# Kernel optimization log

Hardware: AMD Instinct MI355X
Metric: run time of the kernel (lower is better)

## Reference

```python
import jax, jax.numpy as jnp
import numpy as np

D, H, E, K, DFF = 1024, 16, 8, 2, 4096
B, L, T = 4, 512, 2048
EPS = 1e-5


def _xavier(key, shape):
    fan_in, fan_out = shape[-1], shape[-2]
    a = jnp.sqrt(6.0 / (fan_in + fan_out))
    return jax.random.uniform(key, shape, jnp.float32, -a, a)


def setup_inputs() -> dict:
    key = jax.random.key(0)
    ks = jax.random.split(key, 16)
    inp = {
        'latents': jax.random.normal(ks[0], (B, L, D), jnp.float32),
        'tokens': jax.random.normal(ks[1], (B, T, D), jnp.float32),
        # self-attn
        'sa_ln_g': jnp.ones((D,)), 'sa_ln_b': jnp.zeros((D,)),
        'sa_in_w': _xavier(ks[2], (3 * D, D)), 'sa_in_b': jnp.zeros((3 * D,)),
        'sa_out_w': _xavier(ks[3], (D, D)), 'sa_out_b': jnp.zeros((D,)),
        # cross-attn
        'ca_q_ln_g': jnp.ones((D,)), 'ca_q_ln_b': jnp.zeros((D,)),
        'ca_kv_ln_g': jnp.ones((D,)), 'ca_kv_ln_b': jnp.zeros((D,)),
        'ca_in_w': _xavier(ks[4], (3 * D, D)), 'ca_in_b': jnp.zeros((3 * D,)),
        'ca_out_w': _xavier(ks[5], (D, D)), 'ca_out_b': jnp.zeros((D,)),
        # FuseMoE
        'moe_ln_g': jnp.ones((D,)), 'moe_ln_b': jnp.zeros((D,)),
        'router_w': _xavier(ks[6], (E, D)), 'router_b': jnp.zeros((E,)),
        'e_fc1_w': jax.vmap(lambda k: _xavier(k, (DFF, D)))(jax.random.split(ks[7], E)),
        'e_fc1_b': jnp.zeros((E, DFF)),
        'e_fc2_w': jax.vmap(lambda k: _xavier(k, (D, DFF)))(jax.random.split(ks[8], E)),
        'e_fc2_b': jnp.zeros((E, D)),
    }
    return inp


def _ln(x, g, b):
    m = x.mean(-1, keepdims=True)
    v = ((x - m) ** 2).mean(-1, keepdims=True)
    return (x - m) / jnp.sqrt(v + EPS) * g + b


def _mha(q_in, kv_in, in_w, in_b, out_w, out_b):
    # torch nn.MultiheadAttention (batch_first, no masks, eval)
    wq, wk, wv = jnp.split(in_w, 3, axis=0)
    bq, bk, bv = jnp.split(in_b, 3, axis=0)
    dh = D // H
    def heads(x, w, b):  # [B,S,D] -> [B,H,S,dh]
        y = x @ w.T + b
        return y.reshape(x.shape[0], x.shape[1], H, dh).transpose(0, 2, 1, 3)
    q = heads(q_in, wq, bq)
    k = heads(kv_in, wk, bk)
    v = heads(kv_in, wv, bv)
    scores = jnp.einsum('bhqd,bhkd->bhqk', q, k) / jnp.sqrt(jnp.float32(dh))
    attn = jax.nn.softmax(scores, axis=-1)
    out = jnp.einsum('bhqk,bhkd->bhqd', attn, v)
    out = out.transpose(0, 2, 1, 3).reshape(q_in.shape[0], q_in.shape[1], D)
    return out @ out_w.T + out_b


def _fuse_moe(x, ln_g, ln_b, rw, rb, fc1_w, fc1_b, fc2_w, fc2_b):
    h = _ln(x, ln_g, ln_b)
    logits = h @ rw.T + rb                      # [B,L,E]
    vals, idx = jax.lax.top_k(logits, K)        # [B,L,K]
    gates = jax.nn.softmax(vals, axis=-1)
    N = x.shape[0] * x.shape[1]
    hf = h.reshape(N, D)
    # dense all-expert FFN (faithful to original)
    h1 = jax.nn.gelu(jnp.einsum('nd,efd->enf', hf, fc1_w) + fc1_b[:, None, :], approximate=False)
    eo = jnp.einsum('enf,edf->end', h1, fc2_w) + fc2_b[:, None, :]  # [E,N,D]
    idx_f = idx.reshape(N, K)
    gates_f = gates.reshape(N, K)
    gathered = eo[idx_f, jnp.arange(N)[:, None], :]  # [N,K,D]
    mixed = (gathered * gates_f[..., None]).sum(axis=1).reshape(x.shape)
    return x + mixed


def reference(latents, tokens, sa_ln_g, sa_ln_b, sa_in_w, sa_in_b, sa_out_w, sa_out_b,
              ca_q_ln_g, ca_q_ln_b, ca_kv_ln_g, ca_kv_ln_b, ca_in_w, ca_in_b, ca_out_w, ca_out_b,
              moe_ln_g, moe_ln_b, router_w, router_b, e_fc1_w, e_fc1_b, e_fc2_w, e_fc2_b):
    # self-attn (pre-LN, q=k=v)
    q = _ln(latents, sa_ln_g, sa_ln_b)
    x = latents + _mha(q, q, sa_in_w, sa_in_b, sa_out_w, sa_out_b)
    # cross-attn
    qc = _ln(x, ca_q_ln_g, ca_q_ln_b)
    kv = _ln(tokens, ca_kv_ln_g, ca_kv_ln_b)
    x = x + _mha(qc, kv, ca_in_w, ca_in_b, ca_out_w, ca_out_b)
    # FuseMoE FFN
    return _fuse_moe(x, moe_ln_g, moe_ln_b, router_w, router_b, e_fc1_w, e_fc1_b, e_fc2_w, e_fc2_b)
```

## Files before the change

kernel.cpp:

```cpp
#include <hip/hip_runtime.h>
#include <hip/hip_bf16.h>
#include <math.h>

typedef __hip_bfloat16 bf16;
typedef __bf16 bf16x8v __attribute__((ext_vector_type(8)));
typedef float f32x4 __attribute__((ext_vector_type(4)));
typedef unsigned short us8v __attribute__((ext_vector_type(8)));

#define DD   1024
#define HH   16
#define DHD  64
#define EE   8
#define BB   4
#define LL   512
#define TT   2048
#define DFFD 4096
#define NLAT 2048
#define NTOK 8192
#define NASG 4096

__device__ __forceinline__ float toF(float x) { return x; }
__device__ __forceinline__ float toF(bf16 x) { return __bfloat162float(x); }
__device__ __forceinline__ float us2f(unsigned short u) {
    union { unsigned int i; float f; } v; v.i = ((unsigned int)u) << 16; return v.f;
}
__device__ __forceinline__ unsigned short f2us(float f) {
    bf16 t = __float2bfloat16(f);
    return *(unsigned short*)&t;
}

__device__ __forceinline__ float block_sum256(float val, float* red) {
    #pragma unroll
    for (int off = 32; off > 0; off >>= 1) val += __shfl_down(val, off);
    if ((threadIdx.x & 63) == 0) red[threadIdx.x >> 6] = val;
    __syncthreads();
    if (threadIdx.x == 0) red[4] = red[0] + red[1] + red[2] + red[3];
    __syncthreads();
    float r = red[4];
    __syncthreads();
    return r;
}

__global__ __launch_bounds__(256) void ln_kernel(
    const float* __restrict__ x, const float* __restrict__ g, const float* __restrict__ b,
    bf16* __restrict__ out)
{
    __shared__ float red[5];
    int row = blockIdx.x;
    int tid = threadIdx.x;
    const float* xr = x + (size_t)row * DD;
    float v[4];
    #pragma unroll
    for (int i = 0; i < 4; ++i) v[i] = xr[tid + i * 256];
    float s = v[0] + v[1] + v[2] + v[3];
    float mean = block_sum256(s, red) * (1.0f / DD);
    float sq = 0.f;
    #pragma unroll
    for (int i = 0; i < 4; ++i) { float d = v[i] - mean; sq += d * d; }
    float var = block_sum256(sq, red) * (1.0f / DD);
    float rstd = rsqrtf(var + 1e-5f);
    bf16* orow = out + (size_t)row * DD;
    #pragma unroll
    for (int i = 0; i < 4; ++i) {
        int c = tid + i * 256;
        orow[c] = __float2bfloat16((v[i] - mean) * rstd * g[c] + b[c]);
    }
}

template<int SPLIT>
__global__ __launch_bounds__(256) void mfma_gemm_t(
    const bf16* __restrict__ A, const float* __restrict__ W,
    const float* __restrict__ bias,
    bf16* __restrict__ Cb, float* __restrict__ Cf,
    int M, int N, int K,
    const float* __restrict__ res, int act,
    const int* __restrict__ gather,
    const int* __restrict__ seg_off, const int* __restrict__ seg_cnt)
{
    int m_base = 0, mrows = M;
    if (seg_off) {
        int e = blockIdx.z;
        m_base = seg_off[e];
        mrows  = seg_cnt[e];
        W    += (size_t)e * N * K;
        bias += (size_t)e * N;
    }
    const int m0 = blockIdx.y * 128;
    if (m0 >= mrows) return;
    const int n0 = blockIdx.x * 128;

    constexpr int HALF = 4 * 128 * 8;
    __shared__ bf16 smem[(SPLIT ? 3 : 2) * HALF];
    bf16* AsB = smem;
    bf16* WhB = smem + HALF;
    bf16* WlB = smem + 2 * HALF;

    const int tid  = threadIdx.x;
    const int wid  = tid >> 6;
    const int lane = tid & 63;
    const int lg   = lane >> 4;
    const int l16  = lane & 15;
    const int mb   = (wid >> 1) * 64;
    const int nb   = (wid & 1) * 64;

    const int srow  = tid >> 1;
    const int shalf = tid & 1;
    const int kg0   = shalf * 2;

    const bool a_ok = (m0 + srow) < mrows;
    const unsigned short* aptr = nullptr;
    if (a_ok) {
        int grow = m_base + m0 + srow;
        int asrc = gather ? gather[grow] : grow;
        aptr = (const unsigned short*)(A + (size_t)asrc * K + shalf * 16);
    }
    const float* wptr = W + (size_t)(n0 + srow) * K + shalf * 16;

    f32x4 acc[4][4] = {};

    auto load_tile = [&](us8v (&ar)[2], float4 (&wr)[4], int kk) {
        if (a_ok) {
            ar[0] = *(const us8v*)(aptr + kk);
            ar[1] = *(const us8v*)(aptr + kk + 8);
        }
        wr[0] = *(const float4*)(wptr + kk);
        wr[1] = *(const float4*)(wptr + kk + 4);
        wr[2] = *(const float4*)(wptr + kk + 8);
        wr[3] = *(const float4*)(wptr + kk + 12);
    };

    auto store_tile = [&](const us8v (&ar)[2], const float4 (&wr)[4]) {
        *(us8v*)(AsB + ((size_t)kg0 * 128 + srow) * 8)       = ar[0];
        *(us8v*)(AsB + ((size_t)(kg0 + 1) * 128 + srow) * 8) = ar[1];
        const float fw[16] = {wr[0].x, wr[0].y, wr[0].z, wr[0].w,
                              wr[1].x, wr[1].y, wr[1].z, wr[1].w,
                              wr[2].x, wr[2].y, wr[2].z, wr[2].w,
                              wr[3].x, wr[3].y, wr[3].z, wr[3].w};
        us8v hi0, hi1;
        if constexpr (SPLIT) {
            us8v lo0, lo1;
            #pragma unroll
            for (int j = 0; j < 8; ++j) {
                unsigned short h0 = f2us(fw[j]);
                unsigned short h1 = f2us(fw[j + 8]);
                hi0[j] = h0; hi1[j] = h1;
                lo0[j] = f2us(fw[j] - us2f(h0));
                lo1[j] = f2us(fw[j + 8] - us2f(h1));
            }
            *(us8v*)(WlB + ((size_t)kg0 * 128 + srow) * 8)       = lo0;
            *(us8v*)(WlB + ((size_t)(kg0 + 1) * 128 + srow) * 8) = lo1;
        } else {
            #pragma unroll
            for (int j = 0; j < 8; ++j) {
                hi0[j] = f2us(fw[j]);
                hi1[j] = f2us(fw[j + 8]);
            }
        }
        *(us8v*)(WhB + ((size_t)kg0 * 128 + srow) * 8)       = hi0;
        *(us8v*)(WhB + ((size_t)(kg0 + 1) * 128 + srow) * 8) = hi1;
    };

    auto compute = [&]() {
        bf16x8v af[4];
        #pragma unroll
        for (int i = 0; i < 4; ++i)
            af[i] = *(const bf16x8v*)(AsB + ((size_t)lg * 128 + mb + i * 16 + l16) * 8);
        if constexpr (SPLIT) {
            #pragma unroll
            for (int j = 0; j < 4; ++j) {
                bf16x8v wlf = *(const bf16x8v*)(WlB + ((size_t)lg * 128 + nb + j * 16 + l16) * 8);
                #pragma unroll
                for (int i = 0; i < 4; ++i)
                    acc[i][j] = __builtin_amdgcn_mfma_f32_16x16x32_bf16(af[i], wlf, acc[i][j], 0, 0, 0);
            }
        }
        #pragma unroll
        for (int j = 0; j < 4; ++j) {
            bf16x8v wf = *(const bf16x8v*)(WhB + ((size_t)lg * 128 + nb + j * 16 + l16) * 8);
            #pragma unroll
            for (int i = 0; i < 4; ++i)
                acc[i][j] = __builtin_amdgcn_mfma_f32_16x16x32_bf16(af[i], wf, acc[i][j], 0, 0, 0);
        }
    };

    us8v a0[2] = {}, a1[2] = {};
    float4 w0r[4], w1r[4];
    load_tile(a0, w0r, 0);

    for (int k0 = 0; k0 < K; k0 += 64) {
        store_tile(a0, w0r);
        __syncthreads();
        load_tile(a1, w1r, k0 + 32);
        compute();
        __syncthreads();

        store_tile(a1, w1r);
        __syncthreads();
        const int kn = k0 + 64;
        if (kn < K) load_tile(a0, w0r, kn);
        compute();
        __syncthreads();
    }

    #pragma unroll
    for (int i = 0; i < 4; ++i) {
        #pragma unroll
        for (int r = 0; r < 4; ++r) {
            int mm = m0 + mb + i * 16 + lg * 4 + r;
            if (mm >= mrows) continue;
            size_t crow = (size_t)(m_base + mm);
            #pragma unroll
            for (int j = 0; j < 4; ++j) {
                int nn = n0 + nb + j * 16 + l16;
                float v = acc[i][j][r] + bias[nn];
                if (act == 1) v = 0.5f * v * (1.0f + erff(v * 0.70710678118654752f));
                if (res) v += res[crow * (size_t)N + nn];
                if (Cb) Cb[crow * (size_t)N + nn] = __float2bfloat16(v);
                else    Cf[crow * (size_t)N + nn] = v;
            }
        }
    }
}

__global__ __launch_bounds__(256) void attn_mfma_kernel(
    const bf16* __restrict__ Q, int ldq, int qoff,
    const bf16* __restrict__ KV, int ldk, int koff, int voff,
    bf16* __restrict__ O, int Lq, int Tk)
{
    __shared__ bf16 Qs[64][72];
    __shared__ bf16 Ks[32][72];
    __shared__ bf16 Vs[64][40];
    __shared__ bf16 Psh[4][16][40];
    __shared__ bf16 Psl[4][16][40];

    const int nqb = Lq >> 6;
    const int qb  = blockIdx.x % nqb;
    const int h   = (blockIdx.x / nqb) % HH;
    const int b   = blockIdx.x / (nqb * HH);

    const int tid  = threadIdx.x;
    const int wq   = tid >> 6;
    const int lane = tid & 63;
    const int lg   = lane >> 4;
    const int l16  = lane & 15;

    {
        const int row = tid >> 2;
        const int c0  = (tid & 3) * 16;
        const unsigned short* src = (const unsigned short*)
            (Q + (size_t)(b * Lq + qb * 64 + row) * ldq + qoff + h * DHD + c0);
        #pragma unroll
        for (int hf = 0; hf < 2; ++hf) {
            us8v v = *(const us8v*)(src + hf * 8);
            us8v o;
            #pragma unroll
            for (int j = 0; j < 8; ++j) o[j] = f2us(us2f(v[j]) * 0.125f);
            *(us8v*)&Qs[row][c0 + hf * 8] = o;
        }
    }
    __syncthreads();

    const int qrow = wq * 16 + l16;
    const bf16x8v fQ0 = *(const bf16x8v*)&Qs[qrow][lg * 8];
    const bf16x8v fQ1 = *(const bf16x8v*)&Qs[qrow][32 + lg * 8];

    float m = -1e30f, lsum = 0.f;
    f32x4 Of[4] = {};

    const size_t kvbase = (size_t)b * Tk * ldk;
    const int kst_k = tid >> 3;
    const int kst_c = (tid & 7) * 8;
    const int vst_k = (tid & 15) * 2;
    const int vst_d = (tid >> 4) * 4;

    for (int t0 = 0; t0 < Tk; t0 += 32) {
        {
            const bf16* ks = KV + kvbase + (size_t)(t0 + kst_k) * ldk + koff + h * DHD + kst_c;
            *(float4*)&Ks[kst_k][kst_c] = *(const float4*)ks;
        }
        {
            const bf16* vsrc = KV + kvbase + (size_t)(t0 + vst_k) * ldk + voff + h * DHD + vst_d;
            ushort4 a = *(const ushort4*)vsrc;
            ushort4 c = *(const ushort4*)(vsrc + ldk);
            unsigned int w;
            w = (unsigned)a.x | ((unsigned)c.x << 16); *(unsigned*)&Vs[vst_d + 0][vst_k] = w;
            w = (unsigned)a.y | ((unsigned)c.y << 16); *(unsigned*)&Vs[vst_d + 1][vst_k] = w;
            w = (unsigned)a.z | ((unsigned)c.z << 16); *(unsigned*)&Vs[vst_d + 2][vst_k] = w;
            w = (unsigned)a.w | ((unsigned)c.w << 16); *(unsigned*)&Vs[vst_d + 3][vst_k] = w;
        }
        __syncthreads();

        f32x4 st0 = {}, st1 = {};
        {
            const bf16x8v k00 = *(const bf16x8v*)&Ks[l16][lg * 8];
            const bf16x8v k10 = *(const bf16x8v*)&Ks[16 + l16][lg * 8];
            const bf16x8v k01 = *(const bf16x8v*)&Ks[l16][32 + lg * 8];
            const bf16x8v k11 = *(const bf16x8v*)&Ks[16 + l16][32 + lg * 8];
            st0 = __builtin_amdgcn_mfma_f32_16x16x32_bf16(k00, fQ0, st0, 0, 0, 0);
            st1 = __builtin_amdgcn_mfma_f32_16x16x32_bf16(k10, fQ0, st1, 0, 0, 0);
            st0 = __builtin_amdgcn_mfma_f32_16x16x32_bf16(k01, fQ1, st0, 0, 0, 0);
            st1 = __builtin_amdgcn_mfma_f32_16x16x32_bf16(k11, fQ1, st1, 0, 0, 0);
        }

        float cm = fmaxf(fmaxf(fmaxf(st0[0], st0[1]), fmaxf(st0[2], st0[3])),
                         fmaxf(fmaxf(st1[0], st1[1]), fmaxf(st1[2], st1[3])));
        cm = fmaxf(cm, __shfl_xor(cm, 16));
        cm = fmaxf(cm, __shfl_xor(cm, 32));
        const float nm = fmaxf(m, cm);
        float p0[4], p1[4];
        float ps = 0.f;
        #pragma unroll
        for (int r = 0; r < 4; ++r) { p0[r] = expf(st0[r] - nm); ps += p0[r]; }
        #pragma unroll
        for (int r = 0; r < 4; ++r) { p1[r] = expf(st1[r] - nm); ps += p1[r]; }
        ps += __shfl_xor(ps, 16);
        ps += __shfl_xor(ps, 32);
        const float alpha = expf(m - nm);
        lsum = lsum * alpha + ps;
        m = nm;

        ushort4 h0, h1, lo0, lo1;
        #pragma unroll
        for (int r = 0; r < 4; ++r) {
            unsigned short hh = f2us(p0[r]);
            ((unsigned short*)&h0)[r]  = hh;
            ((unsigned short*)&lo0)[r] = f2us(p0[r] - us2f(hh));
        }
        #pragma unroll
        for (int r = 0; r < 4; ++r) {
            unsigned short hh = f2us(p1[r]);
            ((unsigned short*)&h1)[r]  = hh;
            ((unsigned short*)&lo1)[r] = f2us(p1[r] - us2f(hh));
        }
        *(ushort4*)&Psh[wq][l16][lg * 4]      = h0;
        *(ushort4*)&Psh[wq][l16][16 + lg * 4] = h1;
        *(ushort4*)&Psl[wq][l16][lg * 4]      = lo0;
        *(ushort4*)&Psl[wq][l16][16 + lg * 4] = lo1;

        #pragma unroll
        for (int r = 0; r < 4; ++r) {
            const float ar = __shfl(alpha, lg * 4 + r);
            Of[0][r] *= ar; Of[1][r] *= ar; Of[2][r] *= ar; Of[3][r] *= ar;
        }

        __syncthreads();

        const bf16x8v pah = *(const bf16x8v*)&Psh[wq][l16][lg * 8];
        const bf16x8v pal = *(const bf16x8v*)&Psl[wq][l16][lg * 8];
        #pragma unroll
        for (int bb = 0; bb < 4; ++bb) {
            const bf16x8v bv = *(const bf16x8v*)&Vs[bb * 16 + l16][lg * 8];
            Of[bb] = __builtin_amdgcn_mfma_f32_16x16x32_bf16(pal, bv, Of[bb], 0, 0, 0);
            Of[bb] = __builtin_amdgcn_mfma_f32_16x16x32_bf16(pah, bv, Of[bb], 0, 0, 0);
        }
        __syncthreads();
    }

    #pragma unroll
    for (int r = 0; r < 4; ++r) {
        const float inv = 1.0f / __shfl(lsum, lg * 4 + r);
        const int grow = b * Lq + qb * 64 + wq * 16 + lg * 4 + r;
        bf16* orow = O + (size_t)grow * DD + h * DHD;
        #pragma unroll
        for (int bb = 0; bb < 4; ++bb)
            orow[bb * 16 + l16] = __float2bfloat16(Of[bb][r] * inv);
    }
}

__global__ __launch_bounds__(64) void router_kernel(
    const float* __restrict__ X2,
    const float* __restrict__ g, const float* __restrict__ b,
    const float* __restrict__ rw, const float* __restrict__ rb,
    float* __restrict__ gates, int* __restrict__ ebuf, int* __restrict__ counts)
{
    int n = blockIdx.x;
    int lane = threadIdx.x;
    const float* xr = X2 + (size_t)n * DD;

    float v[16];
    #pragma unroll
    for (int i = 0; i < 16; ++i) v[i] = xr[lane + i * 64];

    float s = 0.f;
    #pragma unroll
    for (int i = 0; i < 16; ++i) s += v[i];
    #pragma unroll
    for (int off = 32; off > 0; off >>= 1) s += __shfl_xor(s, off);
    float mean = s * (1.0f / DD);

    float sq = 0.f;
    #pragma unroll
    for (int i = 0; i < 16; ++i) { float d = v[i] - mean; sq += d * d; }
    #pragma unroll
    for (int off = 32; off > 0; off >>= 1) sq += __shfl_xor(sq, off);
    float rstd = rsqrtf(sq * (1.0f / DD) + 1e-5f);

    float h[16];
    #pragma unroll
    for (int i = 0; i < 16; ++i) {
        int c = lane + i * 64;
        h[i] = (v[i] - mean) * rstd * g[c] + b[c];
    }

    float logit[EE];
    #pragma unroll
    for (int e = 0; e < EE; ++e) {
        const float* wr = rw + (size_t)e * DD;
        float p = 0.f;
        #pragma unroll
        for (int i = 0; i < 16; ++i) p += h[i] * wr[lane + i * 64];
        #pragma unroll
        for (int off = 32; off > 0; off >>= 1) p += __shfl_xor(p, off);
        logit[e] = p;
    }

    if (lane == 0) {
        #pragma unroll
        for (int e = 0; e < EE; ++e) logit[e] += rb[e];
        int i0 = 0;
        #pragma unroll
        for (int e = 1; e < EE; ++e) if (logit[e] > logit[i0]) i0 = e;
        int i1 = -1;
        #pragma unroll
        for (int e = 0; e < EE; ++e) {
            if (e == i0) continue;
            if (i1 < 0 || logit[e] > logit[i1]) i1 = e;
        }
        float ex = expf(logit[i1] - logit[i0]);
        float inv = 1.0f / (1.0f + ex);
        gates[2 * n + 0] = inv;
        gates[2 * n + 1] = ex * inv;
        ebuf[2 * n + 0] = i0;
        ebuf[2 * n + 1] = i1;
        atomicAdd(&counts[i0], 1);
        atomicAdd(&counts[i1], 1);
    }
}

__global__ void zero8_kernel(int* __restrict__ p) {
    if (threadIdx.x < EE) p[threadIdx.x] = 0;
}

__global__ void prefix_kernel(const int* __restrict__ counts,
                              int* __restrict__ seg_off, int* __restrict__ cursors) {
    if (threadIdx.x == 0) {
        int acc = 0;
        for (int e = 0; e < EE; ++e) { seg_off[e] = acc; cursors[e] = acc; acc += counts[e]; }
    }
}

__global__ __launch_bounds__(256) void scatter_kernel(
    const int* __restrict__ ebuf, int* __restrict__ cursors,
    int* __restrict__ tok_list, int* __restrict__ r_of)
{
    int n = blockIdx.x * 256 + threadIdx.x;
    if (n < NLAT) {
        for (int k = 0; k < 2; ++k) {
            int e = ebuf[2 * n + k];
            int r = atomicAdd(&cursors[e], 1);
            tok_list[r] = n;
            r_of[2 * n + k] = r;
        }
    }
}

__global__ __launch_bounds__(256) void mix_kernel(
    const float* __restrict__ X2, const bf16* __restrict__ EOUT,
    const float* __restrict__ gates, const int* __restrict__ r_of,
    float* __restrict__ out)
{
    int id = blockIdx.x * 256 + threadIdx.x;
    int n = id >> 10;
    int d = id & 1023;
    float v = X2[id]
            + gates[2 * n + 0] * toF(EOUT[(size_t)r_of[2 * n + 0] * DD + d])
            + gates[2 * n + 1] * toF(EOUT[(size_t)r_of[2 * n + 1] * DD + d]);
    out[id] = v;
}

extern "C" void kernel_launch(void* const* d_in, const int* in_sizes, int n_in,
                              void* d_out, int out_size, void* d_ws, size_t ws_size,
                              hipStream_t stream)
{
    const float* latents  = (const float*)d_in[0];
    const float* tokens   = (const float*)d_in[1];
    const float* sa_ln_g  = (const float*)d_in[2];
    const float* sa_ln_b  = (const float*)d_in[3];
    const float* sa_in_w  = (const float*)d_in[4];
    const float* sa_in_b  = (const float*)d_in[5];
    const float* sa_out_w = (const float*)d_in[6];
    const float* sa_out_b = (const float*)d_in[7];
    const float* ca_q_ln_g  = (const float*)d_in[8];
    const float* ca_q_ln_b  = (const float*)d_in[9];
    const float* ca_kv_ln_g = (const float*)d_in[10];
    const float* ca_kv_ln_b = (const float*)d_in[11];
    const float* ca_in_w  = (const float*)d_in[12];
    const float* ca_in_b  = (const float*)d_in[13];
    const float* ca_out_w = (const float*)d_in[14];
    const float* ca_out_b = (const float*)d_in[15];
    const float* moe_ln_g = (const float*)d_in[16];
    const float* moe_ln_b = (const float*)d_in[17];
    const float* router_w = (const float*)d_in[18];
    const float* router_b = (const float*)d_in[19];
    const float* e_fc1_w  = (const float*)d_in[20];
    const float* e_fc1_b  = (const float*)d_in[21];
    const float* e_fc2_w  = (const float*)d_in[22];
    const float* e_fc2_b  = (const float*)d_in[23];

    char* base = (char*)d_ws;
    const size_t MB = (size_t)1 << 20;
    float* X1   = (float*)(base + 0 * MB);
    float* X2   = (float*)(base + 8 * MB);
    bf16*  H    = (bf16*) (base + 16 * MB);
    bf16*  AO   = (bf16*) (base + 20 * MB);
    bf16*  QCA  = (bf16*) (base + 24 * MB);
    bf16*  KVLN = (bf16*) (base + 28 * MB);
    bf16*  EOUT = (bf16*) (base + 28 * MB);
    bf16*  KVCA = (bf16*) (base + 44 * MB);
    bf16*  QKV  = (bf16*) (base + 44 * MB);
    bf16*  H1   = (bf16*) (base + 44 * MB);
    float* GATES = (float*)(base + 76 * MB);
    int* ebuf     = (int*)(base + 76 * MB + 16384);
    int* tok_list = ebuf + NASG;
    int* r_of     = tok_list + NASG;
    int* counts   = r_of + NASG;
    int* seg_off  = counts + EE;
    int* cursors  = seg_off + EE;

    ln_kernel<<<NLAT, 256, 0, stream>>>(latents, sa_ln_g, sa_ln_b, H);
    {
        dim3 g(3072 / 128, NLAT / 128, 1);
        mfma_gemm_t<1><<<g, 256, 0, stream>>>(H, sa_in_w, sa_in_b, QKV, nullptr,
                                              NLAT, 3072, DD,
                                              nullptr, 0, nullptr, nullptr, nullptr);
    }
    attn_mfma_kernel<<<BB * HH * (LL / 64), 256, 0, stream>>>(
        QKV, 3072, 0, QKV, 3072, 1024, 2048, AO, LL, LL);
    {
        dim3 g(DD / 128, NLAT / 128, 1);
        mfma_gemm_t<1><<<g, 256, 0, stream>>>(AO, sa_out_w, sa_out_b, nullptr, X1,
                                              NLAT, DD, DD,
                                              latents, 0, nullptr, nullptr, nullptr);
    }
    ln_kernel<<<NLAT, 256, 0, stream>>>(X1, ca_q_ln_g, ca_q_ln_b, H);
    ln_kernel<<<NTOK, 256, 0, stream>>>(tokens, ca_kv_ln_g, ca_kv_ln_b, KVLN);
    {
        dim3 g(DD / 128, NLAT / 128, 1);
        mfma_gemm_t<1><<<g, 256, 0, stream>>>(H, ca_in_w, ca_in_b, QCA, nullptr,
                                              NLAT, DD, DD,
                                              nullptr, 0, nullptr, nullptr, nullptr);
    }
    {
        dim3 g(2048 / 128, NTOK / 128, 1);
        mfma_gemm_t<1><<<g, 256, 0, stream>>>(KVLN, ca_in_w + (size_t)1024 * DD, ca_in_b + 1024,
                                              KVCA, nullptr, NTOK, 2048, DD,
                                              nullptr, 0, nullptr, nullptr, nullptr);
    }
    attn_mfma_kernel<<<BB * HH * (LL / 64), 256, 0, stream>>>(
        QCA, 1024, 0, KVCA, 2048, 0, 1024, AO, LL, TT);
    {
        dim3 g(DD / 128, NLAT / 128, 1);
        mfma_gemm_t<1><<<g, 256, 0, stream>>>(AO, ca_out_w, ca_out_b, nullptr, X2,
                                              NLAT, DD, DD,
                                              X1, 0, nullptr, nullptr, nullptr);
    }
    ln_kernel<<<NLAT, 256, 0, stream>>>(X2, moe_ln_g, moe_ln_b, H);
    zero8_kernel<<<1, 64, 0, stream>>>(counts);
    router_kernel<<<NLAT, 64, 0, stream>>>(X2, moe_ln_g, moe_ln_b, router_w, router_b,
                                           GATES, ebuf, counts);
    prefix_kernel<<<1, 64, 0, stream>>>(counts, seg_off, cursors);
    scatter_kernel<<<NLAT / 256, 256, 0, stream>>>(ebuf, cursors, tok_list, r_of);
    {
        dim3 g(DFFD / 128, NLAT / 128, EE);
        mfma_gemm_t<0><<<g, 256, 0, stream>>>(H, e_fc1_w, e_fc1_b, H1, nullptr,
                                              0, DFFD, DD,
                                              nullptr, 1, tok_list, seg_off, counts);
    }
    {
        dim3 g(DD / 128, NLAT / 128, EE);
        mfma_gemm_t<0><<<g, 256, 0, stream>>>(H1, e_fc2_w, e_fc2_b, EOUT, nullptr,
                                              0, DD, DFFD,
                                              nullptr, 0, nullptr, seg_off, counts);
    }
    mix_kernel<<<(NLAT * DD) / 256, 256, 0, stream>>>(X2, EOUT, GATES, r_of, (float*)d_out);
}
```

Before: 1.175 ms.

## Pre-convert expert weights to bf16 and swizzle GEMM workgroups across XCDs

Adds a conversion kernel that casts the fp32 expert FC1/FC2 weights to bf16 in workspace once per call, and adds a GEMM template variant that loads those bf16 weights directly instead of loading fp32 and converting per tile. It also remaps workgroup indices so consecutive tiles land on the same XCD, aiming for better L2 reuse. The conversion pass reads 256MB of fp32 and writes 128MB every call, which may cost more than the per-tile conversion it replaces, since each weight tile is read only by a few M-blocks. The bf16 path runs only when the workspace is large enough.

```diff
diff --git a/kernel.cpp b/kernel.cpp
--- a/kernel.cpp
+++ b/kernel.cpp
@@ -67,9 +67,22 @@
     }
 }
 
-template<int SPLIT>
+__global__ __launch_bounds__(256) void cvt_w_kernel(
+    const float* __restrict__ src, bf16* __restrict__ dst, int n4)
+{
+    const int stride = gridDim.x * 256;
+    for (int i = blockIdx.x * 256 + threadIdx.x; i < n4; i += stride) {
+        float4 v = ((const float4*)src)[i];
+        ushort4 o;
+        o.x = f2us(v.x); o.y = f2us(v.y); o.z = f2us(v.z); o.w = f2us(v.w);
+        ((ushort4*)dst)[i] = o;
+    }
+}
+
+template<int SPLIT, int WB>
 __global__ __launch_bounds__(256) void mfma_gemm_t(
-    const bf16* __restrict__ A, const float* __restrict__ W,
+    const bf16* __restrict__ A, const float* __restrict__ Wf,
+    const bf16* __restrict__ Wb,
     const float* __restrict__ bias,
     bf16* __restrict__ Cb, float* __restrict__ Cf,
     int M, int N, int K,
@@ -82,12 +95,17 @@
         int e = blockIdx.z;
         m_base = seg_off[e];
         mrows  = seg_cnt[e];
-        W    += (size_t)e * N * K;
+        if (WB) Wb += (size_t)e * N * K; else Wf += (size_t)e * N * K;
         bias += (size_t)e * N;
     }
-    const int m0 = blockIdx.y * 128;
+    const int nwg  = gridDim.x * gridDim.y;
+    const int flat = blockIdx.x + gridDim.x * blockIdx.y;
+    const int q8 = nwg >> 3, r8 = nwg & 7;
+    const int xcd = flat & 7, sidx = flat >> 3;
+    const int swz = (xcd < r8 ? xcd * (q8 + 1) : r8 * (q8 + 1) + (xcd - r8) * q8) + sidx;
+    const int n0 = (swz % gridDim.x) * 128;
+    const int m0 = (swz / gridDim.x) * 128;
     if (m0 >= mrows) return;
-    const int n0 = blockIdx.x * 128;
 
     constexpr int HALF = 4 * 128 * 8;
     __shared__ bf16 smem[(SPLIT ? 3 : 2) * HALF];
@@ -114,50 +132,61 @@
         int asrc = gather ? gather[grow] : grow;
         aptr = (const unsigned short*)(A + (size_t)asrc * K + shalf * 16);
     }
-    const float* wptr = W + (size_t)(n0 + srow) * K + shalf * 16;
+    const float* wfptr = WB ? nullptr : (Wf + (size_t)(n0 + srow) * K + shalf * 16);
+    const unsigned short* wbptr = WB ? (const unsigned short*)(Wb + (size_t)(n0 + srow) * K + shalf * 16) : nullptr;
 
     f32x4 acc[4][4] = {};
 
-    auto load_tile = [&](us8v (&ar)[2], float4 (&wr)[4], int kk) {
+    auto load_tile = [&](us8v (&ar)[2], us8v (&wbr)[2], float4 (&wr)[4], int kk) {
         if (a_ok) {
             ar[0] = *(const us8v*)(aptr + kk);
             ar[1] = *(const us8v*)(aptr + kk + 8);
         }
-        wr[0] = *(const float4*)(wptr + kk);
-        wr[1] = *(const float4*)(wptr + kk + 4);
-        wr[2] = *(const float4*)(wptr + kk + 8);
-        wr[3] = *(const float4*)(wptr + kk + 12);
+        if constexpr (WB) {
+            wbr[0] = *(const us8v*)(wbptr + kk);
+            wbr[1] = *(const us8v*)(wbptr + kk + 8);
+        } else {
+            wr[0] = *(const float4*)(wfptr + kk);
+            wr[1] = *(const float4*)(wfptr + kk + 4);
+            wr[2] = *(const float4*)(wfptr + kk + 8);
+            wr[3] = *(const float4*)(wfptr + kk + 12);
+        }
     };
 
-    auto store_tile = [&](const us8v (&ar)[2], const float4 (&wr)[4]) {
+    auto store_tile = [&](const us8v (&ar)[2], const us8v (&wbr)[2], const float4 (&wr)[4]) {
         *(us8v*)(AsB + ((size_t)kg0 * 128 + srow) * 8)       = ar[0];
         *(us8v*)(AsB + ((size_t)(kg0 + 1) * 128 + srow) * 8) = ar[1];
-        const float fw[16] = {wr[0].x, wr[0].y, wr[0].z, wr[0].w,
-                              wr[1].x, wr[1].y, wr[1].z, wr[1].w,
-                              wr[2].x, wr[2].y, wr[2].z, wr[2].w,
-                              wr[3].x, wr[3].y, wr[3].z, wr[3].w};
-        us8v hi0, hi1;
-        if constexpr (SPLIT) {
-            us8v lo0, lo1;
-            #pragma unroll
-            for (int j = 0; j < 8; ++j) {
-                unsigned short h0 = f2us(fw[j]);
-                unsigned short h1 = f2us(fw[j + 8]);
-                hi0[j] = h0; hi1[j] = h1;
-                lo0[j] = f2us(fw[j] - us2f(h0));
-                lo1[j] = f2us(fw[j + 8] - us2f(h1));
+        if constexpr (WB) {
+            *(us8v*)(WhB + ((size_t)kg0 * 128 + srow) * 8)       = wbr[0];
+            *(us8v*)(WhB + ((size_t)(kg0 + 1) * 128 + srow) * 8) = wbr[1];
+        } else {
+            const float fw[16] = {wr[0].x, wr[0].y, wr[0].z, wr[0].w,
+                                  wr[1].x, wr[1].y, wr[1].z, wr[1].w,
+                                  wr[2].x, wr[2].y, wr[2].z, wr[2].w,
+                                  wr[3].x, wr[3].y, wr[3].z, wr[3].w};
+            us8v hi0, hi1;
+            if constexpr (SPLIT) {
+                us8v lo0, lo1;
+                #pragma unroll
+                for (int j = 0; j < 8; ++j) {
+                    unsigned short h0 = f2us(fw[j]);
+                    unsigned short h1 = f2us(fw[j + 8]);
+                    hi0[j] = h0; hi1[j] = h1;
+                    lo0[j] = f2us(fw[j] - us2f(h0));
+                    lo1[j] = f2us(fw[j + 8] - us2f(h1));
+                }
+                *(us8v*)(WlB + ((size_t)kg0 * 128 + srow) * 8)       = lo0;
+                *(us8v*)(WlB + ((size_t)(kg0 + 1) * 128 + srow) * 8) = lo1;
+            } else {
+                #pragma unroll
+                for (int j = 0; j < 8; ++j) {
+                    hi0[j] = f2us(fw[j]);
+                    hi1[j] = f2us(fw[j + 8]);
+                }
             }
-            *(us8v*)(WlB + ((size_t)kg0 * 128 + srow) * 8)       = lo0;
-            *(us8v*)(WlB + ((size_t)(kg0 + 1) * 128 + srow) * 8) = lo1;
-        } else {
-            #pragma unroll
-            for (int j = 0; j < 8; ++j) {
-                hi0[j] = f2us(fw[j]);
-                hi1[j] = f2us(fw[j + 8]);
-            }
-        }
-        *(us8v*)(WhB + ((size_t)kg0 * 128 + srow) * 8)       = hi0;
-        *(us8v*)(WhB + ((size_t)(kg0 + 1) * 128 + srow) * 8) = hi1;
+            *(us8v*)(WhB + ((size_t)kg0 * 128 + srow) * 8)       = hi0;
+            *(us8v*)(WhB + ((size_t)(kg0 + 1) * 128 + srow) * 8) = hi1;
+        }
     };
 
     auto compute = [&]() {
@@ -165,7 +194,7 @@
         #pragma unroll
         for (int i = 0; i < 4; ++i)
             af[i] = *(const bf16x8v*)(AsB + ((size_t)lg * 128 + mb + i * 16 + l16) * 8);
-        if constexpr (SPLIT) {
+        if constexpr (SPLIT && !WB) {
             #pragma unroll
             for (int j = 0; j < 4; ++j) {
                 bf16x8v wlf = *(const bf16x8v*)(WlB + ((size_t)lg * 128 + nb + j * 16 + l16) * 8);
@@ -184,20 +213,21 @@
     };
 
     us8v a0[2] = {}, a1[2] = {};
+    us8v wb0[2] = {}, wb1[2] = {};
     float4 w0r[4], w1r[4];
-    load_tile(a0, w0r, 0);
+    load_tile(a0, wb0, w0r, 0);
 
     for (int k0 = 0; k0 < K; k0 += 64) {
-        store_tile(a0, w0r);
+        store_tile(a0, wb0, w0r);
         __syncthreads();
-        load_tile(a1, w1r, k0 + 32);
+        load_tile(a1, wb1, w1r, k0 + 32);
         compute();
         __syncthreads();
 
-        store_tile(a1, w1r);
+        store_tile(a1, wb1, w1r);
         __syncthreads();
         const int kn = k0 + 64;
-        if (kn < K) load_tile(a0, w0r, kn);
+        if (kn < K) load_tile(a0, wb0, w0r, kn);
         compute();
         __syncthreads();
     }
@@ -526,43 +556,52 @@
     int* counts   = r_of + NASG;
     int* seg_off  = counts + EE;
     int* cursors  = seg_off + EE;
+    bf16* WB1 = (bf16*)(base + 80 * MB);
+    bf16* WB2 = (bf16*)(base + 144 * MB);
+    const bool wb = ws_size >= (size_t)209 * MB;
+
+    if (wb) {
+        cvt_w_kernel<<<2048, 256, 0, stream>>>(e_fc1_w, WB1, (EE * DFFD * DD) / 4);
+        cvt_w_kernel<<<2048, 256, 0, stream>>>(e_fc2_w, WB2, (EE * DD * DFFD) / 4);
+    }
 
     ln_kernel<<<NLAT, 256, 0, stream>>>(latents, sa_ln_g, sa_ln_b, H);
     {
         dim3 g(3072 / 128, NLAT / 128, 1);
-        mfma_gemm_t<1><<<g, 256, 0, stream>>>(H, sa_in_w, sa_in_b, QKV, nullptr,
-                                              NLAT, 3072, DD,
-                                              nullptr, 0, nullptr, nullptr, nullptr);
+        mfma_gemm_t<1, 0><<<g, 256, 0, stream>>>(H, sa_in_w, nullptr, sa_in_b, QKV, nullptr,
+                                                 NLAT, 3072, DD,
+                                                 nullptr, 0, nullptr, nullptr, nullptr);
     }
     attn_mfma_kernel<<<BB * HH * (LL / 64), 256, 0, stream>>>(
         QKV, 3072, 0, QKV, 3072, 1024, 2048, AO, LL, LL);
     {
         dim3 g(DD / 128, NLAT / 128, 1);
-        mfma_gemm_t<1><<<g, 256, 0, stream>>>(AO, sa_out_w, sa_out_b, nullptr, X1,
-                                              NLAT, DD, DD,
-                                              latents, 0, nullptr, nullptr, nullptr);
+        mfma_gemm_t<1, 0><<<g, 256, 0, stream>>>(AO, sa_out_w, nullptr, sa_out_b, nullptr, X1,
+                                                 NLAT, DD, DD,
+                                                 latents, 0, nullptr, nullptr, nullptr);
     }
     ln_kernel<<<NLAT, 256, 0, stream>>>(X1, ca_q_ln_g, ca_q_ln_b, H);
     ln_kernel<<<NTOK, 256, 0, stream>>>(tokens, ca_kv_ln_g, ca_kv_ln_b, KVLN);
     {
         dim3 g(DD / 128, NLAT / 128, 1);
-        mfma_gemm_t<1><<<g, 256, 0, stream>>>(H, ca_in_w, ca_in_b, QCA, nullptr,
-                                              NLAT, DD, DD,
-                                              nullptr, 0, nullptr, nullptr, nullptr);
+        mfma_gemm_t<1, 0><<<g, 256, 0, stream>>>(H, ca_in_w, nullptr, ca_in_b, QCA, nullptr,
+                                                 NLAT, DD, DD,
+                                                 nullptr, 0, nullptr, nullptr, nullptr);
     }
     {
         dim3 g(2048 / 128, NTOK / 128, 1);
-        mfma_gemm_t<1><<<g, 256, 0, stream>>>(KVLN, ca_in_w + (size_t)1024 * DD, ca_in_b + 1024,
-                                              KVCA, nullptr, NTOK, 2048, DD,
-                                              nullptr, 0, nullptr, nullptr, nullptr);
+        mfma_gemm_t<1, 0><<<g, 256, 0, stream>>>(KVLN, ca_in_w + (size_t)1024 * DD, nullptr,
+                                                 ca_in_b + 1024,
+                                                 KVCA, nullptr, NTOK, 2048, DD,
+                                                 nullptr, 0, nullptr, nullptr, nullptr);
     }
     attn_mfma_kernel<<<BB * HH * (LL / 64), 256, 0, stream>>>(
         QCA, 1024, 0, KVCA, 2048, 0, 1024, AO, LL, TT);
     {
         dim3 g(DD / 128, NLAT / 128, 1);
-        mfma_gemm_t<1><<<g, 256, 0, stream>>>(AO, ca_out_w, ca_out_b, nullptr, X2,
-                                              NLAT, DD, DD,
-                                              X1, 0, nullptr, nullptr, nullptr);
+        mfma_gemm_t<1, 0><<<g, 256, 0, stream>>>(AO, ca_out_w, nullptr, ca_out_b, nullptr, X2,
+                                                 NLAT, DD, DD,
+                                                 X1, 0, nullptr, nullptr, nullptr);
     }
     ln_kernel<<<NLAT, 256, 0, stream>>>(X2, moe_ln_g, moe_ln_b, H);
     zero8_kernel<<<1, 64, 0, stream>>>(counts);
@@ -572,15 +611,25 @@
     scatter_kernel<<<NLAT / 256, 256, 0, stream>>>(ebuf, cursors, tok_list, r_of);
     {
         dim3 g(DFFD / 128, NLAT / 128, EE);
-        mfma_gemm_t<0><<<g, 256, 0, stream>>>(H, e_fc1_w, e_fc1_b, H1, nullptr,
-                                              0, DFFD, DD,
-                                              nullptr, 1, tok_list, seg_off, counts);
+        if (wb)
+            mfma_gemm_t<0, 1><<<g, 256, 0, stream>>>(H, nullptr, WB1, e_fc1_b, H1, nullptr,
+                                                     0, DFFD, DD,
+                                                     nullptr, 1, tok_list, seg_off, counts);
+        else
+            mfma_gemm_t<0, 0><<<g, 256, 0, stream>>>(H, e_fc1_w, nullptr, e_fc1_b, H1, nullptr,
+                                                     0, DFFD, DD,
+                                                     nullptr, 1, tok_list, seg_off, counts);
     }
     {
         dim3 g(DD / 128, NLAT / 128, EE);
-        mfma_gemm_t<0><<<g, 256, 0, stream>>>(H1, e_fc2_w, e_fc2_b, EOUT, nullptr,
-                                              0, DD, DFFD,
-                                              nullptr, 0, nullptr, seg_off, counts);
+        if (wb)
+            mfma_gemm_t<0, 1><<<g, 256, 0, stream>>>(H1, nullptr, WB2, e_fc2_b, EOUT, nullptr,
+                                                     0, DD, DFFD,
+                                                     nullptr, 0, nullptr, seg_off, counts);
+        else
+            mfma_gemm_t<0, 0><<<g, 256, 0, stream>>>(H1, e_fc2_w, nullptr, e_fc2_b, EOUT, nullptr,
+                                                     0, DD, DFFD,
+                                                     nullptr, 0, nullptr, seg_off, counts);
     }
     mix_kernel<<<(NLAT * DD) / 256, 256, 0, stream>>>(X2, EOUT, GATES, r_of, (float*)d_out);
 }
```

Result: slower. 1.459 ms (+24.1%).
